# Performance work log

Hardware: AMD Instinct MI355X
Metric: run time of the kernel (lower is better)

Reference implementation:

```python
import jax, jax.numpy as jnp
import numpy as np

ALPHA, GAMMA = 0.25, 2.0
LOC_CW, CLS_CW, OBJ_CW = 1.0, 0.25, 0.1
LOC_W, CLS_W, OBJ_W = 1.0, 1.0, 1.0
B, K, N, C, D = 128, 2048, 4, 64, 3


def _lsa_rows(cost):
    """Hungarian (Kuhn-Munkres with potentials). cost: [n,m], n<=m.
    Returns col assigned to each row (same optimum as scipy.linear_sum_assignment)."""
    cost = np.asarray(cost, dtype=np.float64)
    n, m = cost.shape
    u = np.zeros(n + 1); v = np.zeros(m + 1)
    p = np.zeros(m + 1, dtype=np.int64)
    way = np.zeros(m + 1, dtype=np.int64)
    for i in range(1, n + 1):
        p[0] = i; j0 = 0
        minv = np.full(m + 1, np.inf)
        used = np.zeros(m + 1, dtype=bool)
        while True:
            used[j0] = True
            i0 = p[j0]
            cur = cost[i0 - 1] - u[i0] - v[1:]
            mv = minv[1:]; wy = way[1:]
            free = ~used[1:]
            upd = free & (cur < mv)
            mv[upd] = cur[upd]; wy[upd] = j0
            jrel = np.where(free)[0]
            j1 = jrel[np.argmin(mv[jrel])] + 1
            delta = mv[j1 - 1]
            uj = np.where(used)[0]
            u[p[uj]] += delta
            v[uj] -= delta
            mv[free] -= delta
            j0 = j1
            if p[j0] == 0:
                break
        while j0:
            j1 = way[j0]; p[j0] = p[j1]; j0 = j1
    col_of_row = np.full(n, -1, dtype=np.int64)
    for j in range(1, m + 1):
        if p[j] > 0:
            col_of_row[p[j] - 1] = j - 1
    return col_of_row


def focal_bce(logits, targets, alpha=ALPHA, gamma=GAMMA):
    p = jax.nn.sigmoid(logits)
    # stable BCE-with-logits
    ce = jnp.maximum(logits, 0.0) - logits * targets + jnp.log1p(jnp.exp(-jnp.abs(logits)))
    p_t = p * targets + (1.0 - p) * (1.0 - targets)
    alpha_t = alpha * targets + (1.0 - alpha) * (1.0 - targets)
    return alpha_t * ce * (1.0 - p_t) ** gamma


def _match(loc_out, obj_logit, cls_logit, gt_loc, gt_cls):
    """Hungarian matching (detached, matches torch no_grad block). Returns pred_idx [B,N];
    gt index n is matched to prediction pred_idx[b,n]."""
    eps = 1e-8
    vp = loc_out / jnp.clip(jnp.linalg.norm(loc_out, axis=-1, keepdims=True), eps)
    vt = gt_loc / jnp.clip(jnp.linalg.norm(gt_loc, axis=-1, keepdims=True), eps)
    cos = jnp.clip(jnp.einsum('bkd,bnd->bkn', vp, vt), -1.0 + 1e-6, 1.0 - 1e-6)
    loc_cost = jnp.arccos(cos) / jnp.pi  # [B,K,N]
    # cls cost: focal BCE summed over POSITIVE classes only / pos_count.
    # focal(x, t=1) = alpha * softplus(-x) * (1 - sigmoid(x))**gamma  -> einsum with one-hot gts
    focal_pos = ALPHA * jax.nn.softplus(-cls_logit) * (1.0 - jax.nn.sigmoid(cls_logit)) ** GAMMA  # [B,K,C]
    pos_cnt = jnp.maximum(gt_cls.sum(-1), 1.0)  # [B,N]
    cls_cost = jnp.einsum('bkc,bnc->bkn', focal_pos, gt_cls) / pos_cnt[:, None, :]
    obj_cost = -jax.nn.sigmoid(obj_logit)[:, :, None]  # [B,K,1]
    total = LOC_CW * loc_cost + CLS_CW * cls_cost + OBJ_CW * obj_cost  # [B,K,N]
    total_np = np.asarray(jax.device_get(total))
    # transpose to [N,K] so rows (gt) <= cols (preds)
    pred_idx = np.stack([_lsa_rows(total_np[b].T) for b in range(total_np.shape[0])])
    return jnp.asarray(pred_idx)  # [B,N] int


def _losses(loc_out, obj_logit, cls_logit, gt_loc, gt_cls, pred_idx):
    b, k = loc_out.shape[0], loc_out.shape[1]
    mp_loc = jnp.take_along_axis(loc_out, pred_idx[:, :, None], axis=1)  # [B,N,D]
    mp_cls = jnp.take_along_axis(cls_logit, pred_idx[:, :, None], axis=1)  # [B,N,C]
    # loc criterion = MSE; per-sample mean then /B == global mean (all samples have N>0)
    loc_loss = jnp.mean((mp_loc - gt_loc) ** 2)
    cls_loss = jnp.mean(focal_bce(mp_cls, gt_cls))
    obj_target = jnp.zeros((b, k), dtype=obj_logit.dtype).at[jnp.arange(b)[:, None], pred_idx].set(1.0)
    obj_ce = jnp.maximum(obj_logit, 0.0) - obj_logit * obj_target + jnp.log1p(jnp.exp(-jnp.abs(obj_logit)))
    obj_loss = jnp.mean(obj_ce)
    return LOC_W * loc_loss + CLS_W * cls_loss + OBJ_W * obj_loss


def setup_inputs() -> dict:
    key = jax.random.key(0)
    k1, k2, k3, k4, k5 = jax.random.split(key, 5)
    loc_out = jax.random.normal(k1, (B, K, D), dtype=jnp.float32)
    obj_logit = jax.random.normal(k2, (B, K), dtype=jnp.float32)
    cls_logit = jax.random.normal(k3, (B, K, C), dtype=jnp.float32)
    gt_loc = jax.random.normal(k4, (B, N, D), dtype=jnp.float32)
    cls_idx = jax.random.randint(k5, (B, N), 0, C)
    gt_cls = jax.nn.one_hot(cls_idx, C, dtype=jnp.float32)
    return {'loc_out': loc_out, 'obj_logit': obj_logit, 'cls_logit': cls_logit,
            'gt_loc': gt_loc, 'gt_cls': gt_cls}


def reference(loc_out, obj_logit, cls_logit, gt_loc, gt_cls):
    pred_idx = _match(loc_out, obj_logit, cls_logit, gt_loc, gt_cls)
    return _losses(loc_out, obj_logit, cls_logit, gt_loc, gt_cls, pred_idx)
```

## Files before the change

kernel.cpp:

```cpp
#include <hip/hip_runtime.h>
#include <math.h>
#include <limits.h>

#define BB 128
#define KK 2048
#define NN 4
#define CC 64
#define DD 3
#define SL 16
#define KS (KK/SL)
#define TCOST 128
#define THREADS 256

#define OFF_CVAL 0
#define OFF_CIDX (BB*SL*NN*NN)
#define OFF_OBJ  (2*BB*SL*NN*NN)
#define OFF_PART (OFF_OBJ + BB*SL)

__device__ __forceinline__ float acospi_fast(float x) {
    float ax = fabsf(x);
    float p = ((-0.0187293f*ax + 0.0742610f)*ax - 0.2121144f)*ax + 1.5707288f;
    float r = sqrtf(1.f - ax) * p;
    r = (x >= 0.f) ? r : 3.14159274f - r;
    return r * 0.31830988618379067f;
}

__global__ void __launch_bounds__(TCOST)
crit_cost(const float* __restrict__ loc_out, const float* __restrict__ obj_logit,
          const float* __restrict__ cls_logit, const float* __restrict__ gt_loc,
          const float* __restrict__ gt_cls, float* __restrict__ ws)
{
    __shared__ float cost[NN][KS];
    __shared__ float obj_s[2];

    const int sl  = blockIdx.x;
    const int b   = blockIdx.y;
    const int tid = threadIdx.x;
    const int w   = tid >> 6, lane = tid & 63;
    const int k   = sl*KS + tid;

    const float* lp = loc_out + ((size_t)b*KK + k)*DD;
    float l0 = lp[0], l1 = lp[1], l2 = lp[2];
    float x  = obj_logit[b*KK + k];

    int   cls[NN]; float posin[NN];
    #pragma unroll
    for (int n = 0; n < NN; ++n) {
        float v = gt_cls[(b*NN+n)*CC + lane];
        unsigned long long m = __ballot(v > 0.5f);
        cls[n]   = __ffsll(m) - 1;
        posin[n] = 1.f / fmaxf((float)__popcll(m), 1.f);
    }

    float z[NN];
    #pragma unroll
    for (int n = 0; n < NN; ++n)
        z[n] = cls_logit[((size_t)b*KK + k)*CC + cls[n]];

    float vt[NN][DD];
    #pragma unroll
    for (int n = 0; n < NN; ++n) {
        float g0 = gt_loc[(b*NN+n)*DD+0];
        float g1 = gt_loc[(b*NN+n)*DD+1];
        float g2 = gt_loc[(b*NN+n)*DD+2];
        float gin = 1.f / fmaxf(sqrtf(g0*g0 + g1*g1 + g2*g2), 1e-8f);
        vt[n][0] = g0*gin; vt[n][1] = g1*gin; vt[n][2] = g2*gin;
    }

    float inv = 1.f / fmaxf(sqrtf(l0*l0 + l1*l1 + l2*l2), 1e-8f);
    float v0 = l0*inv, v1 = l1*inv, v2 = l2*inv;
    float obj_base = fmaxf(x, 0.f) + log1pf(expf(-fabsf(x)));
    float oc = -0.1f / (1.f + __expf(-x));
    #pragma unroll
    for (int n = 0; n < NN; ++n) {
        float cosv = v0*vt[n][0] + v1*vt[n][1] + v2*vt[n][2];
        cosv = fminf(fmaxf(cosv, -1.f + 1e-6f), 1.f - 1e-6f);
        float loc_c = acospi_fast(cosv);
        float zz = z[n];
        float e  = __expf(-fabsf(zz));
        float lg = __logf(1.f + e);
        float sp = (zz >= 0.f) ? lg : (lg - zz);
        float r1 = 1.f / (1.f + e);
        float sn = (zz >= 0.f) ? e*r1 : r1;
        float fp = 0.25f * sp * sn * sn;
        cost[n][tid] = loc_c + 0.25f*fp*posin[n] + oc;
    }

    float osum = obj_base;
    #pragma unroll
    for (int off = 32; off > 0; off >>= 1) osum += __shfl_xor(osum, off, 64);
    if (lane == 0) obj_s[w] = osum;
    __syncthreads();

    int* wsi = (int*)ws;
    for (int rr = w; rr < NN; rr += 2) {
        float vv[2]; int gi[2];
        #pragma unroll
        for (int j = 0; j < 2; ++j) {
            vv[j] = cost[rr][lane + 64*j];
            gi[j] = sl*KS + lane + 64*j;
        }
        float cr_val[NN]; int cr_idx[NN];
        #pragma unroll
        for (int r = 0; r < NN; ++r) {
            float bv = vv[0]; int bi = gi[0];
            if (vv[1] < bv || (vv[1] == bv && gi[1] < bi)) { bv = vv[1]; bi = gi[1]; }
            #pragma unroll
            for (int off = 32; off > 0; off >>= 1) {
                float ov = __shfl_xor(bv, off, 64);
                int   oi = __shfl_xor(bi, off, 64);
                if (ov < bv || (ov == bv && oi < bi)) { bv = ov; bi = oi; }
            }
            cr_val[r] = bv; cr_idx[r] = bi;
            #pragma unroll
            for (int j = 0; j < 2; ++j) if (gi[j] == bi) vv[j] = INFINITY;
        }
        if (lane == 0) {
            int base = ((b*SL + sl)*NN + rr)*NN;
            #pragma unroll
            for (int r = 0; r < NN; ++r) {
                ws[OFF_CVAL + base + r]  = cr_val[r];
                wsi[OFF_CIDX + base + r] = cr_idx[r];
            }
        }
    }
    if (tid == 0)
        ws[OFF_OBJ + b*SL + sl] = obj_s[0] + obj_s[1];
}

__global__ void __launch_bounds__(THREADS)
crit_match(const float* __restrict__ loc_out, const float* __restrict__ obj_logit,
           const float* __restrict__ cls_logit, const float* __restrict__ gt_loc,
           const float* __restrict__ gt_cls, float* __restrict__ ws)
{
    __shared__ float cand_val[NN][NN];
    __shared__ int   cand_idx[NN][NN];
    __shared__ int   s_pred[NN];
    __shared__ float s_best[4];
    __shared__ int   s_bestc[4];
    __shared__ float red[4];

    const int b = blockIdx.x, tid = threadIdx.x;
    const int w = tid >> 6, lane = tid & 63;
    const int* wsi = (const int*)ws;

    {
        int sl = lane >> 2, r = lane & 3;
        int base = ((b*SL + sl)*NN + w)*NN + r;
        float v = ws[OFF_CVAL + base];
        int idx = wsi[OFF_CIDX + base];
        #pragma unroll
        for (int r2 = 0; r2 < NN; ++r2) {
            float bv = v; int bi = idx;
            #pragma unroll
            for (int off = 32; off > 0; off >>= 1) {
                float ov = __shfl_xor(bv, off, 64);
                int   oi = __shfl_xor(bi, off, 64);
                if (ov < bv || (ov == bv && oi < bi)) { bv = ov; bi = oi; }
            }
            if (lane == 0) { cand_val[w][r2] = bv; cand_idx[w][r2] = bi; }
            if (idx == bi) v = INFINITY;
        }
    }
    __syncthreads();

    {
        int a0 = (tid >> 6) & 3, a1 = (tid >> 4) & 3, a2 = (tid >> 2) & 3, a3 = tid & 3;
        int c0 = cand_idx[0][a0], c1 = cand_idx[1][a1];
        int c2 = cand_idx[2][a2], c3 = cand_idx[3][a3];
        bool valid = (c0!=c1) & (c0!=c2) & (c0!=c3) & (c1!=c2) & (c1!=c3) & (c2!=c3);
        float t = cand_val[0][a0] + cand_val[1][a1] + cand_val[2][a2] + cand_val[3][a3];
        float bv = valid ? t : INFINITY;
        int   bc = tid;
        #pragma unroll
        for (int off = 32; off > 0; off >>= 1) {
            float ov = __shfl_xor(bv, off, 64);
            int   oc = __shfl_xor(bc, off, 64);
            if (ov < bv || (ov == bv && oc < bc)) { bv = ov; bc = oc; }
        }
        if (lane == 0) { s_best[w] = bv; s_bestc[w] = bc; }
    }
    __syncthreads();

    if (tid == 0) {
        float bv = s_best[0]; int bc = s_bestc[0];
        for (int i = 1; i < 4; ++i)
            if (s_best[i] < bv || (s_best[i] == bv && s_bestc[i] < bc)) { bv = s_best[i]; bc = s_bestc[i]; }
        int a0 = (bc >> 6) & 3, a1 = (bc >> 4) & 3, a2 = (bc >> 2) & 3, a3 = bc & 3;
        s_pred[0] = cand_idx[0][a0]; s_pred[1] = cand_idx[1][a1];
        s_pred[2] = cand_idx[2][a2]; s_pred[3] = cand_idx[3][a3];

        float om = 0.f;
        for (int sl = 0; sl < SL; ++sl) om += ws[OFF_OBJ + b*SL + sl];
        for (int n = 0; n < NN; ++n) om -= obj_logit[b*KK + s_pred[n]];
        ws[OFF_PART + b*3 + 2] = om;

        float s = 0.f;
        for (int n = 0; n < NN; ++n)
            for (int d = 0; d < DD; ++d) {
                float diff = loc_out[((size_t)b*KK + s_pred[n])*DD + d] - gt_loc[(b*NN+n)*DD + d];
                s += diff*diff;
            }
        ws[OFF_PART + b*3 + 0] = s;
    }
    __syncthreads();

    {
        int n = w, c = lane;
        float zz = cls_logit[((size_t)b*KK + s_pred[n])*CC + c];
        float tgt = gt_cls[(b*NN+n)*CC + c];
        float p  = 1.f / (1.f + expf(-zz));
        float ce = fmaxf(zz, 0.f) - zz*tgt + log1pf(expf(-fabsf(zz)));
        float pt = p*tgt + (1.f-p)*(1.f-tgt);
        float at = 0.25f*tgt + 0.75f*(1.f-tgt);
        float om1 = 1.f - pt;
        float r = at * ce * om1 * om1;
        #pragma unroll
        for (int off = 32; off > 0; off >>= 1) r += __shfl_xor(r, off, 64);
        if (lane == 0) red[n] = r;
    }
    __syncthreads();
    if (tid == 0) ws[OFF_PART + b*3 + 1] = red[0] + red[1] + red[2] + red[3];
}

__global__ void __launch_bounds__(BB)
crit_final(const float* __restrict__ ws, float* __restrict__ out)
{
    __shared__ float s2[3][2];
    int t = threadIdx.x;
    int w = t >> 6, lane = t & 63;
    float a = ws[OFF_PART + t*3+0];
    float b = ws[OFF_PART + t*3+1];
    float c = ws[OFF_PART + t*3+2];
    #pragma unroll
    for (int off = 32; off > 0; off >>= 1) {
        a += __shfl_xor(a, off, 64);
        b += __shfl_xor(b, off, 64);
        c += __shfl_xor(c, off, 64);
    }
    if (lane == 0) { s2[0][w] = a; s2[1][w] = b; s2[2][w] = c; }
    __syncthreads();
    if (t == 0) {
        out[0] = (s2[0][0]+s2[0][1]) / (float)(BB*NN*DD)
               + (s2[1][0]+s2[1][1]) / (float)(BB*NN*CC)
               + (s2[2][0]+s2[2][1]) / (float)(BB*KK);
    }
}

extern "C" void kernel_launch(void* const* d_in, const int* in_sizes, int n_in,
                              void* d_out, int out_size, void* d_ws, size_t ws_size,
                              hipStream_t stream) {
    const float* loc_out   = (const float*)d_in[0];
    const float* obj_logit = (const float*)d_in[1];
    const float* cls_logit = (const float*)d_in[2];
    const float* gt_loc    = (const float*)d_in[3];
    const float* gt_cls    = (const float*)d_in[4];
    float* ws  = (float*)d_ws;
    float* out = (float*)d_out;

    hipLaunchKernelGGL(crit_cost, dim3(SL, BB), dim3(TCOST), 0, stream,
                       loc_out, obj_logit, cls_logit, gt_loc, gt_cls, ws);
    hipLaunchKernelGGL(crit_match, dim3(BB), dim3(THREADS), 0, stream,
                       loc_out, obj_logit, cls_logit, gt_loc, gt_cls, ws);
    hipLaunchKernelGGL(crit_final, dim3(1), dim3(BB), 0, stream, ws, out);
}
```

Before: 29.60 us.

## Prune class-logit gathers using lower-bound cost and top-4 threshold

The cost kernel now computes only the location-plus-objectness part of the cost, which is a lower bound because the class term is non-negative. It picks the four lowest bounds per row, gathers their class logits to form exact costs, and uses the largest of these as a threshold. Class logits are then gathered only for candidates whose bound is at or below that threshold. This aims to cut the scattered cls_logit loads, at the price of an extra warp top-4 reduction pass and some divergence.

```diff
diff --git a/kernel.cpp b/kernel.cpp
--- a/kernel.cpp
+++ b/kernel.cpp
@@ -25,12 +25,22 @@
     return r * 0.31830988618379067f;
 }
 
+__device__ __forceinline__ float cls_term_fast(float zz, float posin) {
+    float e  = __expf(-fabsf(zz));
+    float lg = __logf(1.f + e);
+    float sp = (zz >= 0.f) ? lg : (lg - zz);
+    float r1 = 1.f / (1.f + e);
+    float sn = (zz >= 0.f) ? e*r1 : r1;
+    float fp = 0.25f * sp * sn * sn;
+    return 0.25f * fp * posin;
+}
+
 __global__ void __launch_bounds__(TCOST)
 crit_cost(const float* __restrict__ loc_out, const float* __restrict__ obj_logit,
           const float* __restrict__ cls_logit, const float* __restrict__ gt_loc,
           const float* __restrict__ gt_cls, float* __restrict__ ws)
 {
-    __shared__ float cost[NN][KS];
+    __shared__ float lbs[NN][KS];
     __shared__ float obj_s[2];
 
     const int sl  = blockIdx.x;
@@ -51,11 +61,6 @@
         cls[n]   = __ffsll(m) - 1;
         posin[n] = 1.f / fmaxf((float)__popcll(m), 1.f);
     }
-
-    float z[NN];
-    #pragma unroll
-    for (int n = 0; n < NN; ++n)
-        z[n] = cls_logit[((size_t)b*KK + k)*CC + cls[n]];
 
     float vt[NN][DD];
     #pragma unroll
@@ -75,15 +80,7 @@
     for (int n = 0; n < NN; ++n) {
         float cosv = v0*vt[n][0] + v1*vt[n][1] + v2*vt[n][2];
         cosv = fminf(fmaxf(cosv, -1.f + 1e-6f), 1.f - 1e-6f);
-        float loc_c = acospi_fast(cosv);
-        float zz = z[n];
-        float e  = __expf(-fabsf(zz));
-        float lg = __logf(1.f + e);
-        float sp = (zz >= 0.f) ? lg : (lg - zz);
-        float r1 = 1.f / (1.f + e);
-        float sn = (zz >= 0.f) ? e*r1 : r1;
-        float fp = 0.25f * sp * sn * sn;
-        cost[n][tid] = loc_c + 0.25f*fp*posin[n] + oc;
+        lbs[n][tid] = acospi_fast(cosv) + oc;
     }
 
     float osum = obj_base;
@@ -92,35 +89,76 @@
     if (lane == 0) obj_s[w] = osum;
     __syncthreads();
 
+    const float* zrow = cls_logit + (size_t)b*KK*CC;
     int* wsi = (int*)ws;
+
     for (int rr = w; rr < NN; rr += 2) {
-        float vv[2]; int gi[2];
+        const int   cl = cls[rr];
+        const float pi_ = posin[rr];
+
+        float m0 = lbs[rr][lane], m1 = lbs[rr][lane+64];
+        int   i0 = lane,          i1 = lane+64;
+        float seedv[4]; int seedl[4];
         #pragma unroll
-        for (int j = 0; j < 2; ++j) {
-            vv[j] = cost[rr][lane + 64*j];
-            gi[j] = sl*KS + lane + 64*j;
-        }
-        float cr_val[NN]; int cr_idx[NN];
-        #pragma unroll
-        for (int r = 0; r < NN; ++r) {
-            float bv = vv[0]; int bi = gi[0];
-            if (vv[1] < bv || (vv[1] == bv && gi[1] < bi)) { bv = vv[1]; bi = gi[1]; }
+        for (int r = 0; r < 4; ++r) {
+            float bv = m0; int bi = i0;
+            if (m1 < bv || (m1 == bv && i1 < bi)) { bv = m1; bi = i1; }
             #pragma unroll
             for (int off = 32; off > 0; off >>= 1) {
                 float ov = __shfl_xor(bv, off, 64);
                 int   oi = __shfl_xor(bi, off, 64);
                 if (ov < bv || (ov == bv && oi < bi)) { bv = ov; bi = oi; }
             }
-            cr_val[r] = bv; cr_idx[r] = bi;
+            seedv[r] = bv; seedl[r] = bi;
+            if (i0 == bi) m0 = INFINITY;
+            if (i1 == bi) m1 = INFINITY;
+        }
+
+        {
+            int j  = lane & 3;
+            int kl = seedl[j];
+            float zz = zrow[(size_t)(sl*KS + kl)*CC + cl];
+            float ts = seedv[j] + cls_term_fast(zz, pi_);
+            float t0 = __shfl(ts, 0, 64), t1 = __shfl(ts, 1, 64);
+            float t2 = __shfl(ts, 2, 64), t3 = __shfl(ts, 3, 64);
+            float tau = fmaxf(fmaxf(t0, t1), fmaxf(t2, t3));
+
+            float ev[2]; int gidx[2];
             #pragma unroll
-            for (int j = 0; j < 2; ++j) if (gi[j] == bi) vv[j] = INFINITY;
-        }
-        if (lane == 0) {
-            int base = ((b*SL + sl)*NN + rr)*NN;
+            for (int j2 = 0; j2 < 2; ++j2) {
+                int kl2 = lane + 64*j2;
+                float lbv = lbs[rr][kl2];
+                float tot = INFINITY;
+                if (lbv <= tau) {
+                    float z2 = zrow[(size_t)(sl*KS + kl2)*CC + cl];
+                    tot = lbv + cls_term_fast(z2, pi_);
+                }
+                ev[j2]   = tot;
+                gidx[j2] = sl*KS + kl2;
+            }
+
+            float cr_val[NN]; int cr_idx[NN];
             #pragma unroll
-            for (int r = 0; r < NN; ++r) {
-                ws[OFF_CVAL + base + r]  = cr_val[r];
-                wsi[OFF_CIDX + base + r] = cr_idx[r];
+            for (int r = 0; r < 4; ++r) {
+                float bv = ev[0]; int bi = gidx[0];
+                if (ev[1] < bv || (ev[1] == bv && gidx[1] < bi)) { bv = ev[1]; bi = gidx[1]; }
+                #pragma unroll
+                for (int off = 32; off > 0; off >>= 1) {
+                    float ov = __shfl_xor(bv, off, 64);
+                    int   oi = __shfl_xor(bi, off, 64);
+                    if (ov < bv || (ov == bv && oi < bi)) { bv = ov; bi = oi; }
+                }
+                cr_val[r] = bv; cr_idx[r] = bi;
+                if (gidx[0] == bi) ev[0] = INFINITY;
+                if (gidx[1] == bi) ev[1] = INFINITY;
+            }
+            if (lane == 0) {
+                int base = ((b*SL + sl)*NN + rr)*NN;
+                #pragma unroll
+                for (int r = 0; r < NN; ++r) {
+                    ws[OFF_CVAL + base + r]  = cr_val[r];
+                    wsi[OFF_CIDX + base + r] = cr_idx[r];
+                }
             }
         }
     }
```

New measurement: 29.69 us. No clear change (+0.3%).
